# Kernel tuning notes

Measured on AMD Instinct MI355X. Metric: run time of the kernel, lower is better.

## Reference

```python
import jax, jax.numpy as jnp
import numpy as np

N = 50000          # nodes
E = 800000         # edges (before self-loops)
IN_CH = 16
HID = 32
HEADS = 4
NEG_SLOPE = 0.2    # PyG GATConv default leaky_relu slope


def add_self_loops(edge_index, n):
    loops = jnp.arange(n, dtype=edge_index.dtype)
    return jnp.concatenate([edge_index, jnp.stack([loops, loops])], axis=1)


def gat_layer(x, edge_index, W, a_src, a_dst, bias, heads, out_ch, concat):
    """PyG-style GATConv: gather -> attention logits -> segment softmax over dst -> scatter."""
    n = x.shape[0]
    h = (x @ W).reshape(n, heads, out_ch)            # [N, H, C]
    src, dst = edge_index[0], edge_index[1]          # messages flow src -> dst
    alpha_src = (h * a_src).sum(-1)                  # [N, H]
    alpha_dst = (h * a_dst).sum(-1)                  # [N, H]
    e = jax.nn.leaky_relu(alpha_src[src] + alpha_dst[dst], NEG_SLOPE)  # [Etot, H]
    # numerically stable segment softmax over incoming edges of each dst node
    e_max = jax.ops.segment_max(e, dst, num_segments=n)
    e_exp = jnp.exp(e - e_max[dst])
    denom = jax.ops.segment_sum(e_exp, dst, num_segments=n)
    alpha = e_exp / (denom[dst] + 1e-16)             # [Etot, H]
    out = jax.ops.segment_sum(h[src] * alpha[..., None], dst, num_segments=n)  # [N, H, C]
    out = out.reshape(n, heads * out_ch) if concat else out.mean(axis=1)
    return out + bias


def setup_inputs() -> dict:
    key = jax.random.key(0)
    ks = jax.random.split(key, 10)
    x = jax.random.normal(ks[0], (N, IN_CH), dtype=jnp.float32)
    edge_index = jax.random.randint(ks[1], (2, E), 0, N, dtype=jnp.int64)
    s = 0.1
    W1 = jax.random.normal(ks[2], (IN_CH, HEADS * HID), dtype=jnp.float32) * s
    a_src1 = jax.random.normal(ks[3], (1, HEADS, HID), dtype=jnp.float32) * s
    a_dst1 = jax.random.normal(ks[4], (1, HEADS, HID), dtype=jnp.float32) * s
    b1 = jnp.zeros((HEADS * HID,), dtype=jnp.float32)
    W2 = jax.random.normal(ks[5], (HEADS * HID, 2), dtype=jnp.float32) * s
    a_src2 = jax.random.normal(ks[6], (1, 1, 2), dtype=jnp.float32) * s
    a_dst2 = jax.random.normal(ks[7], (1, 1, 2), dtype=jnp.float32) * s
    b2 = jnp.zeros((2,), dtype=jnp.float32)
    return {"x": x, "edge_index": edge_index,
            "W1": W1, "a_src1": a_src1, "a_dst1": a_dst1, "b1": b1,
            "W2": W2, "a_src2": a_src2, "a_dst2": a_dst2, "b2": b2}


def reference(x, edge_index, W1, a_src1, a_dst1, b1, W2, a_src2, a_dst2, b2):
    ei = add_self_loops(edge_index, x.shape[0])
    h = gat_layer(x, ei, W1, a_src1, a_dst1, b1, HEADS, HID, concat=True)
    h = jax.nn.relu(h)
    out = gat_layer(h, ei, W2, a_src2, a_dst2, b2, 1, 2, concat=False)
    return out
```

## Files before the change

kernel.cpp:

```cpp
#include <hip/hip_runtime.h>
#include <hip/hip_bf16.h>

#define N_NODES 50000
#define N_EDGES 800000
#define ETOT    (N_EDGES + N_NODES)
#define STRIDE  64
#define IN_CH   16
#define HID     32
#define HEADS   4
#define C1      (HEADS * HID)
#define NEG     0.2f

#define DEG_BLOCKS ((ETOT / 4 + 255) / 256)
#define H1_BLOCKS  (N_NODES / 4)

typedef unsigned short u16;
typedef unsigned int   u32;

__device__ __forceinline__ float bf2f(u16 b) {
    return __uint_as_float(((u32)b) << 16);
}

__device__ __forceinline__ u16 f2bf(float f) {
    __hip_bfloat16 hb = __float2bfloat16(f);
    return *(u16*)&hb;
}

__device__ __forceinline__ int clampn(int v) {
    return v < 0 ? 0 : (v >= N_NODES ? N_NODES - 1 : v);
}

__device__ __forceinline__ int eidx(const int* ei, int e, int i64, int which) {
    int v = i64 ? ei[2 * (which * N_EDGES + e)] : ei[which * N_EDGES + e];
    return clampn(v);
}

__device__ __forceinline__ float cvt(const void* src, int i, int bf) {
    return bf ? bf2f(((const u16*)src)[i]) : ((const float*)src)[i];
}

__device__ __forceinline__ int probe_bf_wave(const u16* xb) {
    int l = threadIdx.x & 63;
    int my = 0;
#pragma unroll
    for (int k = 0; k < 4; k++) {
        float f = bf2f(xb[l * 4 + k]);
        float a = fabsf(f);
        if (f == 0.0f || (a > 9.5e-7f && a < 1.05e6f)) my++;
    }
#pragma unroll
    for (int m = 32; m; m >>= 1) my += __shfl_xor(my, m);
    return my >= 224;
}

__device__ __forceinline__ int probe_i64_wave(const int* ei32) {
    int l = threadIdx.x & 63;
    int nz = (l < 32 && ei32[2 * l + 1] != 0) ? 1 : 0;
#pragma unroll
    for (int m = 32; m; m >>= 1) nz += __shfl_xor(nz, m);
    return nz == 0;
}


__device__ __forceinline__ void dev_deg(const int* __restrict__ ei,
                                        int* __restrict__ degs,
                                        u32* __restrict__ srp, int blk) {
    int i64 = probe_i64_wave(ei);
    int e0 = (blk * 256 + (int)threadIdx.x) * 4;
    if (e0 >= ETOT) return;
    int s[4], d[4];
#pragma unroll
    for (int j = 0; j < 4; j++) {
        int e = e0 + j;
        if (e < N_EDGES) { s[j] = eidx(ei, e, i64, 0); d[j] = eidx(ei, e, i64, 1); }
        else             { s[j] = d[j] = e - N_EDGES; }
    }
    u32 r[4];
#pragma unroll
    for (int j = 0; j < 4; j++) {
        u32 rr = (u32)atomicAdd(&degs[d[j]], 1);
        r[j] = ((u32)s[j] << 16) | (rr > 0xFFFFu ? 0xFFFFu : rr);
    }
    *(uint4*)(srp + e0) = make_uint4(r[0], r[1], r[2], r[3]);
}

__device__ __forceinline__ void dev_h1(const void* __restrict__ x,
                                       const void* __restrict__ W1,
                                       const void* __restrict__ a_s,
                                       const void* __restrict__ a_d,
                                       u32* __restrict__ h1u,
                                       float* __restrict__ as1,
                                       float* __restrict__ ad1,
                                       float* Ws, float* As, float* Ad,
                                       float (*xs)[IN_CH], int blk) {
    int bf = probe_bf_wave((const u16*)x);
    if (blk == 0 && threadIdx.x < 4) as1[N_NODES * 4 + threadIdx.x] = -1e30f;
    for (int i = threadIdx.x; i < IN_CH * C1 + 2 * C1; i += 256) {
        if (i < IN_CH * C1)           Ws[i] = cvt(W1, i, bf);
        else if (i < IN_CH * C1 + C1) As[i - IN_CH * C1] = cvt(a_s, i - IN_CH * C1, bf);
        else                          Ad[i - IN_CH * C1 - C1] = cvt(a_d, i - IN_CH * C1 - C1, bf);
    }
    int w = threadIdx.x >> 6, l = threadIdx.x & 63;
    int n = blk * 4 + w;
    if (l < IN_CH) xs[w][l] = cvt(x, n * IN_CH + l, bf);
    __syncthreads();

    int c0 = 2 * l, c1 = 2 * l + 1;
    float acc0 = 0.f, acc1 = 0.f;
#pragma unroll
    for (int k = 0; k < IN_CH; k++) {
        float xv = xs[w][k];
        acc0 += xv * Ws[k * C1 + c0];
        acc1 += xv * Ws[k * C1 + c1];
    }
    h1u[n * 64 + l] = (u32)f2bf(acc0) | ((u32)f2bf(acc1) << 16);

    float ps = acc0 * As[c0] + acc1 * As[c1];
    float pd = acc0 * Ad[c0] + acc1 * Ad[c1];
#pragma unroll
    for (int m = 8; m; m >>= 1) { ps += __shfl_xor(ps, m); pd += __shfl_xor(pd, m); }
    if ((l & 15) == 0) {
        int hd = l >> 4;
        as1[n * 4 + hd] = ps;
        ad1[n * 4 + hd] = pd;
    }
}

__launch_bounds__(256)
__global__ void k_build(const void* __restrict__ x, const int* __restrict__ ei,
                        const void* __restrict__ W1, const void* __restrict__ a_s,
                        const void* __restrict__ a_d,
                        int* __restrict__ degs, u32* __restrict__ srp,
                        u32* __restrict__ h1u, float* __restrict__ as1,
                        float* __restrict__ ad1) {
    __shared__ float Ws[IN_CH * C1];
    __shared__ float As[C1], Ad[C1];
    __shared__ float xs[4][IN_CH];
    if (blockIdx.x < DEG_BLOCKS) { dev_deg(ei, degs, srp, blockIdx.x); return; }
    dev_h1(x, W1, a_s, a_d, h1u, as1, ad1, Ws, As, Ad, xs, blockIdx.x - DEG_BLOCKS);
}

__launch_bounds__(256)
__global__ void k_deg_only(const int* __restrict__ ei, int* __restrict__ degs,
                           u32* __restrict__ srp) {
    dev_deg(ei, degs, srp, blockIdx.x);
}

__launch_bounds__(256)
__global__ void k_h1_only(const void* __restrict__ x, const void* __restrict__ W1,
                          const void* __restrict__ a_s, const void* __restrict__ a_d,
                          u32* __restrict__ h1u, float* __restrict__ as1,
                          float* __restrict__ ad1) {
    __shared__ float Ws[IN_CH * C1];
    __shared__ float As[C1], Ad[C1];
    __shared__ float xs[4][IN_CH];
    dev_h1(x, W1, a_s, a_d, h1u, as1, ad1, Ws, As, Ad, xs, blockIdx.x);
}

__launch_bounds__(256)
__global__ void k_fill(const int* __restrict__ ei, const u32* __restrict__ srp,
                       u16* __restrict__ csr) {
    int i64 = probe_i64_wave(ei);
    int e0 = (blockIdx.x * 256 + (int)threadIdx.x) * 4;
    if (e0 >= ETOT) return;
    uint4 q = *(const uint4*)(srp + e0);
    u32 sr[4] = {q.x, q.y, q.z, q.w};
#pragma unroll
    for (int j = 0; j < 4; j++) {
        int e = e0 + j;
        int d = (e < N_EDGES) ? eidx(ei, e, i64, 1) : (e - N_EDGES);
        u32 r = sr[j] & 0xFFFFu;
        if (r < STRIDE) csr[d * STRIDE + r] = (u16)(sr[j] >> 16);
    }
}

__launch_bounds__(256)
__global__ void k_gather1(const void* __restrict__ x,
                          const int* __restrict__ degs, const u16* __restrict__ csr,
                          const u32* __restrict__ h1u,
                          const float* __restrict__ as1, const float* __restrict__ ad1,
                          const void* __restrict__ b1, const void* __restrict__ W2,
                          const void* __restrict__ a2s, const void* __restrict__ a2d,
                          float* __restrict__ h2, float* __restrict__ as2,
                          float* __restrict__ ad2) {
    int bf = probe_bf_wave((const u16*)x);
    int n = blockIdx.x * 4 + (threadIdx.x >> 6);
    int l = threadIdx.x & 63;
    int hd = l >> 4;
    int jb = l & 15;
    float adv = ad1[n * 4 + hd];
    int deg = degs[n]; deg = deg > STRIDE ? STRIDE : deg;
    int nb = (deg + 15) >> 4;
    const u16* row = csr + (size_t)n * STRIDE;
    float acc0 = 0.f, acc1 = 0.f, sw = 0.f;

    for (int b = 0; b < nb; b++) {
        int se = (int)row[b * 16 + jb];
        if (se >= N_NODES) se = N_NODES;
        float t = as1[se * 4 + hd] + adv;
        t = t > 0.f ? t : NEG * t;
        float wm = __expf(t);
#pragma unroll
        for (int j = 0; j < 16; j++) {
            int   sj = __shfl(se, j);
            float wj = __shfl(wm, hd * 16 + j);
            u32 p = h1u[sj * 64 + l];
            sw   += wj;
            acc0 += wj * bf2f((u16)(p & 0xFFFF));
            acc1 += wj * bf2f((u16)(p >> 16));
        }
    }

    float inv = 1.0f / sw;
    float v0 = acc0 * inv + cvt(b1, 2 * l, bf);
    float v1 = acc1 * inv + cvt(b1, 2 * l + 1, bf);
    v0 = v0 > 0.f ? v0 : 0.f;
    v1 = v1 > 0.f ? v1 : 0.f;
    float p0 = v0 * cvt(W2, 4 * l,     bf) + v1 * cvt(W2, 4 * l + 2, bf);
    float p1 = v0 * cvt(W2, 4 * l + 1, bf) + v1 * cvt(W2, 4 * l + 3, bf);
#pragma unroll
    for (int d = 32; d; d >>= 1) { p0 += __shfl_down(p0, d); p1 += __shfl_down(p1, d); }
    if (l == 0) {
        h2[n * 2] = p0; h2[n * 2 + 1] = p1;
        as2[n] = p0 * cvt(a2s, 0, bf) + p1 * cvt(a2s, 1, bf);
        ad2[n] = p0 * cvt(a2d, 0, bf) + p1 * cvt(a2d, 1, bf);
    }
}

__launch_bounds__(256)
__global__ void k_gather2(const void* __restrict__ x,
                          const int* __restrict__ degs, const u16* __restrict__ csr,
                          const float* __restrict__ h2, const float* __restrict__ as2,
                          const float* __restrict__ ad2, const void* __restrict__ b2,
                          void* __restrict__ out) {
    int bf = probe_bf_wave((const u16*)x);
    int n = blockIdx.x * 16 + (threadIdx.x >> 4);
    int g = threadIdx.x & 15;
    float adv = ad2[n], a0 = 0.f, a1 = 0.f, sw = 0.f;
    int deg = degs[n]; deg = deg > STRIDE ? STRIDE : deg;
    const u16* row = csr + (size_t)n * STRIDE;
    for (int k = g; k < deg; k += 16) {
        int s = (int)row[k];
        float lg = as2[s] + adv;
        lg = lg > 0.f ? lg : NEG * lg;
        float w = __expf(lg);
        float2 hv = ((const float2*)h2)[s];
        a0 += w * hv.x;
        a1 += w * hv.y;
        sw += w;
    }
#pragma unroll
    for (int m = 8; m; m >>= 1) {
        a0 += __shfl_xor(a0, m); a1 += __shfl_xor(a1, m); sw += __shfl_xor(sw, m);
    }
    if (g == 0) {
        float inv = 1.0f / sw;
        float o0 = a0 * inv + cvt(b2, 0, bf);
        float o1 = a1 * inv + cvt(b2, 1, bf);
        if (bf) {
            ((u32*)out)[n] = (u32)f2bf(o0) | ((u32)f2bf(o1) << 16);
        } else {
            ((float2*)out)[n] = make_float2(o0, o1);
        }
    }
}

extern "C" void kernel_launch(void* const* d_in, const int* in_sizes, int n_in,
                              void* d_out, int out_size, void* d_ws, size_t ws_size,
                              hipStream_t stream) {
    const void* x    = d_in[0];
    const int*  ei   = (const int*)d_in[1];
    const void* W1   = d_in[2];
    const void* a_s1 = d_in[3];
    const void* a_d1 = d_in[4];
    const void* b1   = d_in[5];
    const void* W2   = d_in[6];
    const void* a_s2 = d_in[7];
    const void* a_d2 = d_in[8];
    const void* b2   = d_in[9];

    char* p = (char*)d_ws;
    int*   degs = (int*)p;     p += ((size_t)N_NODES * 4 + 255) & ~255;
    u16*   csr  = (u16*)p;     p += (size_t)N_NODES * STRIDE * 2;
    u32*   h1u  = (u32*)p;     p += (size_t)(N_NODES + 1) * 64 * 4;
    float* as1  = (float*)p;   p += (size_t)(N_NODES + 1) * HEADS * 4;
    float* ad1  = (float*)p;   p += (size_t)N_NODES * HEADS * 4;
    float* h2   = (float*)p;   p += (size_t)N_NODES * 2 * 4;
    float* as2  = (float*)p;   p += (size_t)N_NODES * 4;
    float* ad2  = (float*)p;   p += (size_t)N_NODES * 4;
    size_t base_used = (size_t)(p - (char*)d_ws);
    size_t srp_bytes = (size_t)ETOT * 4;

    hipMemsetAsync(degs, 0, (size_t)N_NODES * sizeof(int), stream);
    hipMemsetAsync(csr, 0xFF, (size_t)N_NODES * STRIDE * 2, stream);

    if (ws_size >= base_used + srp_bytes) {
        u32* srp = (u32*)p;
        k_build<<<DEG_BLOCKS + H1_BLOCKS, 256, 0, stream>>>(
            x, ei, W1, a_s1, a_d1, degs, srp, h1u, as1, ad1);
        k_fill<<<DEG_BLOCKS, 256, 0, stream>>>(ei, srp, csr);
    } else {
        u32* srp = h1u;
        k_deg_only<<<DEG_BLOCKS, 256, 0, stream>>>(ei, degs, srp);
        k_fill<<<DEG_BLOCKS, 256, 0, stream>>>(ei, srp, csr);
        k_h1_only<<<H1_BLOCKS, 256, 0, stream>>>(x, W1, a_s1, a_d1, h1u, as1, ad1);
    }
    k_gather1<<<N_NODES / 4, 256, 0, stream>>>(
        x, degs, csr, h1u, as1, ad1, b1, W2, a_s2, a_d2, h2, as2, ad2);
    k_gather2<<<N_NODES / 16, 256, 0, stream>>>(
        x, degs, csr, h2, as2, ad2, b2, d_out);
}
```

Baseline: 216.1 us.

## Co-schedule CSR fill with grid-strided h1 projection; load weights once per block

Moves the node projection (x@W1 plus attention logits) out of the degree-counting kernel and into the CSR fill kernel, so the atomic-heavy degree pass runs alone and the fill pass overlaps with the projection. The projection now uses a fixed grid of 2048 blocks that loop over node groups, so the shared-memory weight staging is paid once per block instead of once per group of 4 nodes. It also adds a typed fast path for the weight loads and broadcasts x through wave shuffles instead of shared memory. The risk is less parallelism per block in the projection, and the kernel boundaries are reshuffled.

```diff
diff --git a/kernel.cpp b/kernel.cpp
--- a/kernel.cpp
+++ b/kernel.cpp
@@ -12,7 +12,8 @@
 #define NEG     0.2f
 
 #define DEG_BLOCKS ((ETOT / 4 + 255) / 256)
-#define H1_BLOCKS  (N_NODES / 4)
+#define NGROUPS    (N_NODES / 4)
+#define H1_BLOCKS  2048
 
 typedef unsigned short u16;
 typedef unsigned int   u32;
@@ -60,7 +61,6 @@
     for (int m = 32; m; m >>= 1) nz += __shfl_xor(nz, m);
     return nz == 0;
 }
-
 
 __device__ __forceinline__ void dev_deg(const int* __restrict__ ei,
                                         int* __restrict__ degs,
@@ -84,6 +84,23 @@
     *(uint4*)(srp + e0) = make_uint4(r[0], r[1], r[2], r[3]);
 }
 
+__device__ __forceinline__ void dev_fill(const int* __restrict__ ei,
+                                         const u32* __restrict__ srp,
+                                         u16* __restrict__ csr, int blk) {
+    int i64 = probe_i64_wave(ei);
+    int e0 = (blk * 256 + (int)threadIdx.x) * 4;
+    if (e0 >= ETOT) return;
+    uint4 q = *(const uint4*)(srp + e0);
+    u32 sr[4] = {q.x, q.y, q.z, q.w};
+#pragma unroll
+    for (int j = 0; j < 4; j++) {
+        int e = e0 + j;
+        int d = (e < N_EDGES) ? eidx(ei, e, i64, 1) : (e - N_EDGES);
+        u32 r = sr[j] & 0xFFFFu;
+        if (r < STRIDE) csr[d * STRIDE + r] = (u16)(sr[j] >> 16);
+    }
+}
+
 __device__ __forceinline__ void dev_h1(const void* __restrict__ x,
                                        const void* __restrict__ W1,
                                        const void* __restrict__ a_s,
@@ -91,59 +108,82 @@
                                        u32* __restrict__ h1u,
                                        float* __restrict__ as1,
                                        float* __restrict__ ad1,
-                                       float* Ws, float* As, float* Ad,
-                                       float (*xs)[IN_CH], int blk) {
+                                       float* Ws, float* As, float* Ad, int blk) {
     int bf = probe_bf_wave((const u16*)x);
     if (blk == 0 && threadIdx.x < 4) as1[N_NODES * 4 + threadIdx.x] = -1e30f;
-    for (int i = threadIdx.x; i < IN_CH * C1 + 2 * C1; i += 256) {
-        if (i < IN_CH * C1)           Ws[i] = cvt(W1, i, bf);
-        else if (i < IN_CH * C1 + C1) As[i - IN_CH * C1] = cvt(a_s, i - IN_CH * C1, bf);
-        else                          Ad[i - IN_CH * C1 - C1] = cvt(a_d, i - IN_CH * C1 - C1, bf);
-    }
+    if (bf) {
+        const u32* w32 = (const u32*)W1;
+        for (int i = threadIdx.x; i < IN_CH * C1 / 2; i += 256) {
+            u32 v = w32[i];
+            Ws[2 * i]     = bf2f((u16)(v & 0xFFFF));
+            Ws[2 * i + 1] = bf2f((u16)(v >> 16));
+        }
+        const u32* s32 = (const u32*)a_s;
+        const u32* d32 = (const u32*)a_d;
+        for (int i = threadIdx.x; i < C1 / 2; i += 256) {
+            u32 vs = s32[i], vd = d32[i];
+            As[2 * i]     = bf2f((u16)(vs & 0xFFFF));
+            As[2 * i + 1] = bf2f((u16)(vs >> 16));
+            Ad[2 * i]     = bf2f((u16)(vd & 0xFFFF));
+            Ad[2 * i + 1] = bf2f((u16)(vd >> 16));
+        }
+    } else {
+        for (int i = threadIdx.x; i < IN_CH * C1; i += 256) Ws[i] = ((const float*)W1)[i];
+        for (int i = threadIdx.x; i < C1; i += 256) {
+            As[i] = ((const float*)a_s)[i];
+            Ad[i] = ((const float*)a_d)[i];
+        }
+    }
+    __syncthreads();
+
     int w = threadIdx.x >> 6, l = threadIdx.x & 63;
-    int n = blk * 4 + w;
-    if (l < IN_CH) xs[w][l] = cvt(x, n * IN_CH + l, bf);
-    __syncthreads();
-
     int c0 = 2 * l, c1 = 2 * l + 1;
-    float acc0 = 0.f, acc1 = 0.f;
-#pragma unroll
-    for (int k = 0; k < IN_CH; k++) {
-        float xv = xs[w][k];
-        acc0 += xv * Ws[k * C1 + c0];
-        acc1 += xv * Ws[k * C1 + c1];
-    }
-    h1u[n * 64 + l] = (u32)f2bf(acc0) | ((u32)f2bf(acc1) << 16);
-
-    float ps = acc0 * As[c0] + acc1 * As[c1];
-    float pd = acc0 * Ad[c0] + acc1 * Ad[c1];
-#pragma unroll
-    for (int m = 8; m; m >>= 1) { ps += __shfl_xor(ps, m); pd += __shfl_xor(pd, m); }
-    if ((l & 15) == 0) {
-        int hd = l >> 4;
-        as1[n * 4 + hd] = ps;
-        ad1[n * 4 + hd] = pd;
-    }
-}
-
-__launch_bounds__(256)
-__global__ void k_build(const void* __restrict__ x, const int* __restrict__ ei,
-                        const void* __restrict__ W1, const void* __restrict__ a_s,
-                        const void* __restrict__ a_d,
-                        int* __restrict__ degs, u32* __restrict__ srp,
-                        u32* __restrict__ h1u, float* __restrict__ as1,
-                        float* __restrict__ ad1) {
+    for (int g = blk; g < NGROUPS; g += H1_BLOCKS) {
+        int n = g * 4 + w;
+        float xval = (l < IN_CH) ? cvt(x, n * IN_CH + l, bf) : 0.f;
+        float acc0 = 0.f, acc1 = 0.f;
+#pragma unroll
+        for (int k = 0; k < IN_CH; k++) {
+            float xk = __shfl(xval, k);
+            acc0 += xk * Ws[k * C1 + c0];
+            acc1 += xk * Ws[k * C1 + c1];
+        }
+        h1u[n * 64 + l] = (u32)f2bf(acc0) | ((u32)f2bf(acc1) << 16);
+
+        float ps = acc0 * As[c0] + acc1 * As[c1];
+        float pd = acc0 * Ad[c0] + acc1 * Ad[c1];
+#pragma unroll
+        for (int m = 8; m; m >>= 1) { ps += __shfl_xor(ps, m); pd += __shfl_xor(pd, m); }
+        if ((l & 15) == 0) {
+            int hd = l >> 4;
+            as1[n * 4 + hd] = ps;
+            ad1[n * 4 + hd] = pd;
+        }
+    }
+}
+
+__launch_bounds__(256)
+__global__ void k_deg(const int* __restrict__ ei, int* __restrict__ degs,
+                      u32* __restrict__ srp) {
+    dev_deg(ei, degs, srp, blockIdx.x);
+}
+
+__launch_bounds__(256)
+__global__ void k_fill_h1(const void* __restrict__ x, const int* __restrict__ ei,
+                          const void* __restrict__ W1, const void* __restrict__ a_s,
+                          const void* __restrict__ a_d, const u32* __restrict__ srp,
+                          u16* __restrict__ csr, u32* __restrict__ h1u,
+                          float* __restrict__ as1, float* __restrict__ ad1) {
     __shared__ float Ws[IN_CH * C1];
     __shared__ float As[C1], Ad[C1];
-    __shared__ float xs[4][IN_CH];
-    if (blockIdx.x < DEG_BLOCKS) { dev_deg(ei, degs, srp, blockIdx.x); return; }
-    dev_h1(x, W1, a_s, a_d, h1u, as1, ad1, Ws, As, Ad, xs, blockIdx.x - DEG_BLOCKS);
-}
-
-__launch_bounds__(256)
-__global__ void k_deg_only(const int* __restrict__ ei, int* __restrict__ degs,
-                           u32* __restrict__ srp) {
-    dev_deg(ei, degs, srp, blockIdx.x);
+    if (blockIdx.x < DEG_BLOCKS) { dev_fill(ei, srp, csr, blockIdx.x); return; }
+    dev_h1(x, W1, a_s, a_d, h1u, as1, ad1, Ws, As, Ad, blockIdx.x - DEG_BLOCKS);
+}
+
+__launch_bounds__(256)
+__global__ void k_fill(const int* __restrict__ ei, const u32* __restrict__ srp,
+                       u16* __restrict__ csr) {
+    dev_fill(ei, srp, csr, blockIdx.x);
 }
 
 __launch_bounds__(256)
@@ -153,25 +193,7 @@
                           float* __restrict__ ad1) {
     __shared__ float Ws[IN_CH * C1];
     __shared__ float As[C1], Ad[C1];
-    __shared__ float xs[4][IN_CH];
-    dev_h1(x, W1, a_s, a_d, h1u, as1, ad1, Ws, As, Ad, xs, blockIdx.x);
-}
-
-__launch_bounds__(256)
-__global__ void k_fill(const int* __restrict__ ei, const u32* __restrict__ srp,
-                       u16* __restrict__ csr) {
-    int i64 = probe_i64_wave(ei);
-    int e0 = (blockIdx.x * 256 + (int)threadIdx.x) * 4;
-    if (e0 >= ETOT) return;
-    uint4 q = *(const uint4*)(srp + e0);
-    u32 sr[4] = {q.x, q.y, q.z, q.w};
-#pragma unroll
-    for (int j = 0; j < 4; j++) {
-        int e = e0 + j;
-        int d = (e < N_EDGES) ? eidx(ei, e, i64, 1) : (e - N_EDGES);
-        u32 r = sr[j] & 0xFFFFu;
-        if (r < STRIDE) csr[d * STRIDE + r] = (u16)(sr[j] >> 16);
-    }
+    dev_h1(x, W1, a_s, a_d, h1u, as1, ad1, Ws, As, Ad, blockIdx.x);
 }
 
 __launch_bounds__(256)
@@ -296,12 +318,12 @@
 
     if (ws_size >= base_used + srp_bytes) {
         u32* srp = (u32*)p;
-        k_build<<<DEG_BLOCKS + H1_BLOCKS, 256, 0, stream>>>(
-            x, ei, W1, a_s1, a_d1, degs, srp, h1u, as1, ad1);
-        k_fill<<<DEG_BLOCKS, 256, 0, stream>>>(ei, srp, csr);
+        k_deg<<<DEG_BLOCKS, 256, 0, stream>>>(ei, degs, srp);
+        k_fill_h1<<<DEG_BLOCKS + H1_BLOCKS, 256, 0, stream>>>(
+            x, ei, W1, a_s1, a_d1, srp, csr, h1u, as1, ad1);
     } else {
         u32* srp = h1u;
-        k_deg_only<<<DEG_BLOCKS, 256, 0, stream>>>(ei, degs, srp);
+        k_deg<<<DEG_BLOCKS, 256, 0, stream>>>(ei, degs, srp);
         k_fill<<<DEG_BLOCKS, 256, 0, stream>>>(ei, srp, csr);
         k_h1_only<<<H1_BLOCKS, 256, 0, stream>>>(x, W1, a_s1, a_d1, h1u, as1, ad1);
     }
```

After: 208.8 us. -3.4%, faster.
